# Performance work log

Measured on AMD Instinct MI355X. Metric: run time of the kernel, lower is better.

The kernel has to match this reference:

```python
import jax, jax.numpy as jnp
import numpy as np
from jax import lax

B, C, H, W = 32, 256, 56, 56
K = 3  # kernel_size

def setup_inputs() -> dict:
    key = jax.random.key(0)
    k1, k2, k3 = jax.random.split(key, 3)
    x = jax.random.normal(k1, (B, C, H, W), dtype=jnp.float32)
    # 1x1 conv weight Conv2d(C, C*K*K, 1) flattened to a linear map [C*K*K, C]
    Wk = jax.random.normal(k2, (C * K * K, C), dtype=jnp.float32) * 0.02
    bk = jax.random.normal(k3, (C * K * K,), dtype=jnp.float32) * 0.02
    return {"x": x, "Wk": Wk, "bk": bk}

def reference(x, Wk, bk):
    b, c, h, w = x.shape
    # kernel generator: global avg pool -> 1x1 conv -> relu
    pooled = x.mean(axis=(2, 3))                       # [B, C]
    kern = jax.nn.relu(pooled @ Wk.T + bk)             # [B, C*K*K]
    kern = kern.reshape(b * c, 1, K, K)                # OIHW, one filter per (b,c)
    # per-sample, per-channel depthwise conv: groups = B*C
    xr = x.reshape(1, b * c, h, w)
    out = lax.conv_general_dilated(
        xr, kern,
        window_strides=(1, 1),
        padding=[(K // 2, K // 2), (K // 2, K // 2)],
        feature_group_count=b * c,
        dimension_numbers=("NCHW", "OIHW", "NCHW"),
    )
    return out.reshape(b, c, h, w)
```

## Files before the change

kernel.cpp:

```cpp
#include <hip/hip_runtime.h>

#define B_  32
#define C_  256
#define H_  56
#define W_  56
#define HW  3136
#define KK  9
#define OC  2304
#define NPLANES (B_*C_)

typedef float v4f __attribute__((ext_vector_type(4)));

__global__ __launch_bounds__(256) void pool_kernel(const float* __restrict__ x,
                                                   float* __restrict__ pooled) {
    const int wid  = threadIdx.x >> 6;
    const int lane = threadIdx.x & 63;
    const int plane = blockIdx.x * 4 + wid;
    const float4* xp = (const float4*)(x + (size_t)plane * HW);

    float s = 0.f;
    #pragma unroll
    for (int k = 0; k < 12; ++k) {
        float4 v = xp[lane + k * 64];
        s += (v.x + v.y) + (v.z + v.w);
    }
    if (lane < 16) {
        float4 v = xp[768 + lane];
        s += (v.x + v.y) + (v.z + v.w);
    }
    #pragma unroll
    for (int off = 32; off > 0; off >>= 1)
        s += __shfl_down(s, off, 64);
    if (lane == 0)
        pooled[plane] = s * (1.0f / (float)HW);
}

__global__ __launch_bounds__(256) void kgen_kernel(const float* __restrict__ pooled,
                                                   const float* __restrict__ Wk,
                                                   const float* __restrict__ bk,
                                                   float* __restrict__ kern) {
    const int b = blockIdx.x / 9;
    const int g = blockIdx.x % 9;
    __shared__ float p[C_];
    p[threadIdx.x] = pooled[b * C_ + threadIdx.x];
    __syncthreads();

    const int o = g * 256 + threadIdx.x;
    const float4* wrow = (const float4*)(Wk + (size_t)o * C_);
    const float4* pv   = (const float4*)p;
    float acc = 0.f;
    #pragma unroll 4
    for (int i = 0; i < C_ / 4; ++i) {
        float4 w = wrow[i];
        float4 q = pv[i];
        acc += w.x * q.x + w.y * q.y + w.z * q.z + w.w * q.w;
    }
    acc += bk[o];
    kern[(size_t)b * OC + o] = fmaxf(acc, 0.f);
}

__global__ __launch_bounds__(256) void dconv_kernel(const float* __restrict__ x,
                                                    const float* __restrict__ kern,
                                                    float* __restrict__ out) {
    const int plane = blockIdx.x;
    __shared__ float lds[58 * 58];
    const int t = threadIdx.x;

    const float4* xp = (const float4*)(x + (size_t)plane * HW);
    float4 v0 = xp[t];
    float4 v1 = xp[t + 256];
    float4 v2 = xp[t + 512];
    float4 v3 = make_float4(0.f, 0.f, 0.f, 0.f);
    if (t < 16) v3 = xp[t + 768];

    if (t < 58) { lds[t] = 0.f; lds[57 * 58 + t] = 0.f; }
    if (t < 56) { lds[(t + 1) * 58] = 0.f; lds[(t + 1) * 58 + 57] = 0.f; }

    {
        int s, r, c0, base;
        s = t;        r = s / 14; c0 = (s % 14) * 4; base = (r + 1) * 58 + c0 + 1;
        lds[base] = v0.x; lds[base + 1] = v0.y; lds[base + 2] = v0.z; lds[base + 3] = v0.w;
        s = t + 256;  r = s / 14; c0 = (s % 14) * 4; base = (r + 1) * 58 + c0 + 1;
        lds[base] = v1.x; lds[base + 1] = v1.y; lds[base + 2] = v1.z; lds[base + 3] = v1.w;
        s = t + 512;  r = s / 14; c0 = (s % 14) * 4; base = (r + 1) * 58 + c0 + 1;
        lds[base] = v2.x; lds[base + 1] = v2.y; lds[base + 2] = v2.z; lds[base + 3] = v2.w;
        if (t < 16) {
            s = t + 768; r = s / 14; c0 = (s % 14) * 4; base = (r + 1) * 58 + c0 + 1;
            lds[base] = v3.x; lds[base + 1] = v3.y; lds[base + 2] = v3.z; lds[base + 3] = v3.w;
        }
    }

    const float* kw = kern + (size_t)plane * KK;
    const float w0 = kw[0], w1 = kw[1], w2 = kw[2],
                w3 = kw[3], w4 = kw[4], w5 = kw[5],
                w6 = kw[6], w7 = kw[7], w8 = kw[8];

    __syncthreads();

    float* op = out + (size_t)plane * HW;

    auto do_strip = [&](int s) {
        const int r  = s / 14;
        const int c0 = (s % 14) * 4;
        const float* R0 = &lds[(r + 0) * 58 + c0];
        const float* R1 = &lds[(r + 1) * 58 + c0];
        const float* R2 = &lds[(r + 2) * 58 + c0];
        float2 q00 = *(const float2*)(R0),     q01 = *(const float2*)(R0 + 2), q02 = *(const float2*)(R0 + 4);
        float2 q10 = *(const float2*)(R1),     q11 = *(const float2*)(R1 + 2), q12 = *(const float2*)(R1 + 4);
        float2 q20 = *(const float2*)(R2),     q21 = *(const float2*)(R2 + 2), q22 = *(const float2*)(R2 + 4);
        const float a0 = q00.x, a1 = q00.y, a2 = q01.x, a3 = q01.y, a4 = q02.x, a5 = q02.y;
        const float b0 = q10.x, b1 = q10.y, b2 = q11.x, b3 = q11.y, b4 = q12.x, b5 = q12.y;
        const float c0f = q20.x, c1 = q20.y, c2 = q21.x, c3 = q21.y, c4 = q22.x, c5 = q22.y;
        v4f res;
        res.x = a0*w0 + a1*w1 + a2*w2 + b0*w3 + b1*w4 + b2*w5 + c0f*w6 + c1*w7 + c2*w8;
        res.y = a1*w0 + a2*w1 + a3*w2 + b1*w3 + b2*w4 + b3*w5 + c1*w6 + c2*w7 + c3*w8;
        res.z = a2*w0 + a3*w1 + a4*w2 + b2*w3 + b3*w4 + b4*w5 + c2*w6 + c3*w7 + c4*w8;
        res.w = a3*w0 + a4*w1 + a5*w2 + b3*w3 + b4*w4 + b5*w5 + c3*w6 + c4*w7 + c5*w8;
        __builtin_nontemporal_store(res, (v4f*)op + s);
    };

    do_strip(t);
    do_strip(t + 256);
    do_strip(t + 512);
    if (t < 16) do_strip(t + 768);
}

extern "C" void kernel_launch(void* const* d_in, const int* in_sizes, int n_in,
                              void* d_out, int out_size, void* d_ws, size_t ws_size,
                              hipStream_t stream) {
    const float* x  = (const float*)d_in[0];
    const float* Wk = (const float*)d_in[1];
    const float* bk = (const float*)d_in[2];
    float* out = (float*)d_out;

    float* pooled = (float*)d_ws;
    float* kern   = pooled + NPLANES;

    pool_kernel<<<NPLANES / 4, 256, 0, stream>>>(x, pooled);
    kgen_kernel<<<B_ * 9, 256, 0, stream>>>(pooled, Wk, bk, kern);
    dconv_kernel<<<NPLANES, 256, 0, stream>>>(x, kern, out);
}
```

Measured before the change: 212.6 us.

## Fuse kernel generation into depthwise conv and compute two output rows per thread

Removes the separate kernel-generation launch. Each conv block now computes its own 9 filter taps from pooled means and Wk, using 144 threads with a 16-lane shuffle reduction, and keeps them in shared memory. The conv loop also now produces two vertically adjacent output rows per thread, so overlapping rows read from LDS are reused. The cost is extra Wk reads per block (9 rows of 256 floats) and a different thread work split, where some threads do two iterations.

```diff
diff --git a/kernel.cpp b/kernel.cpp
--- a/kernel.cpp
+++ b/kernel.cpp
@@ -35,35 +35,16 @@
         pooled[plane] = s * (1.0f / (float)HW);
 }
 
-__global__ __launch_bounds__(256) void kgen_kernel(const float* __restrict__ pooled,
-                                                   const float* __restrict__ Wk,
-                                                   const float* __restrict__ bk,
-                                                   float* __restrict__ kern) {
-    const int b = blockIdx.x / 9;
-    const int g = blockIdx.x % 9;
-    __shared__ float p[C_];
-    p[threadIdx.x] = pooled[b * C_ + threadIdx.x];
-    __syncthreads();
-
-    const int o = g * 256 + threadIdx.x;
-    const float4* wrow = (const float4*)(Wk + (size_t)o * C_);
-    const float4* pv   = (const float4*)p;
-    float acc = 0.f;
-    #pragma unroll 4
-    for (int i = 0; i < C_ / 4; ++i) {
-        float4 w = wrow[i];
-        float4 q = pv[i];
-        acc += w.x * q.x + w.y * q.y + w.z * q.z + w.w * q.w;
-    }
-    acc += bk[o];
-    kern[(size_t)b * OC + o] = fmaxf(acc, 0.f);
-}
-
 __global__ __launch_bounds__(256) void dconv_kernel(const float* __restrict__ x,
-                                                    const float* __restrict__ kern,
+                                                    const float* __restrict__ pooled,
+                                                    const float* __restrict__ Wk,
+                                                    const float* __restrict__ bk,
                                                     float* __restrict__ out) {
     const int plane = blockIdx.x;
+    const int b = plane >> 8;
+    const int c = plane & 255;
     __shared__ float lds[58 * 58];
+    __shared__ float wsh[KK];
     const int t = threadIdx.x;
 
     const float4* xp = (const float4*)(x + (size_t)plane * HW);
@@ -72,6 +53,26 @@
     float4 v2 = xp[t + 512];
     float4 v3 = make_float4(0.f, 0.f, 0.f, 0.f);
     if (t < 16) v3 = xp[t + 768];
+
+    if (t < 144) {
+        const int o  = t >> 4;
+        const int ch = (t & 15) << 4;
+        const int og = c * KK + o;
+        const float4* wr = (const float4*)(Wk + (size_t)og * C_ + ch);
+        const float4* pr = (const float4*)(pooled + b * C_ + ch);
+        float s = 0.f;
+        #pragma unroll
+        for (int i = 0; i < 4; ++i) {
+            float4 w = wr[i];
+            float4 p = pr[i];
+            s += w.x * p.x + w.y * p.y + w.z * p.z + w.w * p.w;
+        }
+        #pragma unroll
+        for (int off = 8; off > 0; off >>= 1)
+            s += __shfl_down(s, off, 16);
+        if ((t & 15) == 0)
+            wsh[o] = fmaxf(s + bk[og], 0.f);
+    }
 
     if (t < 58) { lds[t] = 0.f; lds[57 * 58 + t] = 0.f; }
     if (t < 56) { lds[(t + 1) * 58] = 0.f; lds[(t + 1) * 58 + 57] = 0.f; }
@@ -90,39 +91,43 @@
         }
     }
 
-    const float* kw = kern + (size_t)plane * KK;
-    const float w0 = kw[0], w1 = kw[1], w2 = kw[2],
-                w3 = kw[3], w4 = kw[4], w5 = kw[5],
-                w6 = kw[6], w7 = kw[7], w8 = kw[8];
+    __syncthreads();
 
-    __syncthreads();
+    const float w0 = wsh[0], w1 = wsh[1], w2 = wsh[2],
+                w3 = wsh[3], w4 = wsh[4], w5 = wsh[5],
+                w6 = wsh[6], w7 = wsh[7], w8 = wsh[8];
 
     float* op = out + (size_t)plane * HW;
 
-    auto do_strip = [&](int s) {
-        const int r  = s / 14;
-        const int c0 = (s % 14) * 4;
-        const float* R0 = &lds[(r + 0) * 58 + c0];
-        const float* R1 = &lds[(r + 1) * 58 + c0];
-        const float* R2 = &lds[(r + 2) * 58 + c0];
-        float2 q00 = *(const float2*)(R0),     q01 = *(const float2*)(R0 + 2), q02 = *(const float2*)(R0 + 4);
-        float2 q10 = *(const float2*)(R1),     q11 = *(const float2*)(R1 + 2), q12 = *(const float2*)(R1 + 4);
-        float2 q20 = *(const float2*)(R2),     q21 = *(const float2*)(R2 + 2), q22 = *(const float2*)(R2 + 4);
-        const float a0 = q00.x, a1 = q00.y, a2 = q01.x, a3 = q01.y, a4 = q02.x, a5 = q02.y;
-        const float b0 = q10.x, b1 = q10.y, b2 = q11.x, b3 = q11.y, b4 = q12.x, b5 = q12.y;
-        const float c0f = q20.x, c1 = q20.y, c2 = q21.x, c3 = q21.y, c4 = q22.x, c5 = q22.y;
-        v4f res;
-        res.x = a0*w0 + a1*w1 + a2*w2 + b0*w3 + b1*w4 + b2*w5 + c0f*w6 + c1*w7 + c2*w8;
-        res.y = a1*w0 + a2*w1 + a3*w2 + b1*w3 + b2*w4 + b3*w5 + c1*w6 + c2*w7 + c3*w8;
-        res.z = a2*w0 + a3*w1 + a4*w2 + b2*w3 + b3*w4 + b4*w5 + c2*w6 + c3*w7 + c4*w8;
-        res.w = a3*w0 + a4*w1 + a5*w2 + b3*w3 + b4*w4 + b5*w5 + c3*w6 + c4*w7 + c5*w8;
-        __builtin_nontemporal_store(res, (v4f*)op + s);
-    };
+    for (int i = t; i < 392; i += 256) {
+        const int rp = i / 14;
+        const int c0 = (i % 14) * 4;
+        const float* R0 = &lds[(2 * rp + 0) * 58 + c0];
+        const float* R1 = &lds[(2 * rp + 1) * 58 + c0];
+        const float* R2 = &lds[(2 * rp + 2) * 58 + c0];
+        const float* R3 = &lds[(2 * rp + 3) * 58 + c0];
+        float2 p0 = *(const float2*)(R0), p1 = *(const float2*)(R0 + 2), p2 = *(const float2*)(R0 + 4);
+        float2 q0 = *(const float2*)(R1), q1 = *(const float2*)(R1 + 2), q2 = *(const float2*)(R1 + 4);
+        float2 r0 = *(const float2*)(R2), r1 = *(const float2*)(R2 + 2), r2 = *(const float2*)(R2 + 4);
+        float2 s0 = *(const float2*)(R3), s1 = *(const float2*)(R3 + 2), s2 = *(const float2*)(R3 + 4);
+        const float a0 = p0.x, a1 = p0.y, a2 = p1.x, a3 = p1.y, a4 = p2.x, a5 = p2.y;
+        const float b0 = q0.x, b1 = q0.y, b2 = q1.x, b3 = q1.y, b4 = q2.x, b5 = q2.y;
+        const float c0f = r0.x, c1f = r0.y, c2f = r1.x, c3f = r1.y, c4f = r2.x, c5f = r2.y;
+        const float d0 = s0.x, d1 = s0.y, d2 = s1.x, d3 = s1.y, d4 = s2.x, d5 = s2.y;
 
-    do_strip(t);
-    do_strip(t + 256);
-    do_strip(t + 512);
-    if (t < 16) do_strip(t + 768);
+        v4f t0, t1;
+        t0.x = a0*w0 + a1*w1 + a2*w2 + b0*w3 + b1*w4 + b2*w5 + c0f*w6 + c1f*w7 + c2f*w8;
+        t0.y = a1*w0 + a2*w1 + a3*w2 + b1*w3 + b2*w4 + b3*w5 + c1f*w6 + c2f*w7 + c3f*w8;
+        t0.z = a2*w0 + a3*w1 + a4*w2 + b2*w3 + b3*w4 + b4*w5 + c2f*w6 + c3f*w7 + c4f*w8;
+        t0.w = a3*w0 + a4*w1 + a5*w2 + b3*w3 + b4*w4 + b5*w5 + c3f*w6 + c4f*w7 + c5f*w8;
+        t1.x = b0*w0 + b1*w1 + b2*w2 + c0f*w3 + c1f*w4 + c2f*w5 + d0*w6 + d1*w7 + d2*w8;
+        t1.y = b1*w0 + b2*w1 + b3*w2 + c1f*w3 + c2f*w4 + c3f*w5 + d1*w6 + d2*w7 + d3*w8;
+        t1.z = b2*w0 + b3*w1 + b4*w2 + c2f*w3 + c3f*w4 + c4f*w5 + d2*w6 + d3*w7 + d4*w8;
+        t1.w = b3*w0 + b4*w1 + b5*w2 + c3f*w3 + c4f*w4 + c5f*w5 + d3*w6 + d4*w7 + d5*w8;
+
+        __builtin_nontemporal_store(t0, (v4f*)(op + (2 * rp + 0) * W_ + c0));
+        __builtin_nontemporal_store(t1, (v4f*)(op + (2 * rp + 1) * W_ + c0));
+    }
 }
 
 extern "C" void kernel_launch(void* const* d_in, const int* in_sizes, int n_in,
@@ -134,9 +139,7 @@
     float* out = (float*)d_out;
 
     float* pooled = (float*)d_ws;
-    float* kern   = pooled + NPLANES;
 
     pool_kernel<<<NPLANES / 4, 256, 0, stream>>>(x, pooled);
-    kgen_kernel<<<B_ * 9, 256, 0, stream>>>(pooled, Wk, bk, kern);
-    dconv_kernel<<<NPLANES, 256, 0, stream>>>(x, kern, out);
+    dconv_kernel<<<NPLANES, 256, 0, stream>>>(x, pooled, Wk, bk, out);
 }
```

Measured after the change: 200.1 us (median of 2 runs). 5.9% less time.
